# Performance work log

Measured on AMD Instinct MI355X. Metric: run time of the kernel, lower is better.

## Reference

```python
import jax, jax.numpy as jnp
import numpy as np

BATCH, D_MODEL, N_STATE, SEQ_L = 8, 1024, 64, 2048


def setup_inputs() -> dict:
    key = jax.random.key(0)
    k_u, k_a, k_b, k_c = jax.random.split(key, 4)
    scale = 1.0 / (D_MODEL * N_STATE) ** 0.5
    u = jax.random.normal(k_u, (BATCH, D_MODEL, SEQ_L), dtype=jnp.float32)
    # A is stored as a full NxN diagonal matrix, as in the torch module
    A = jnp.diag(jax.random.uniform(k_a, (N_STATE,), dtype=jnp.float32))
    B = jax.random.normal(k_b, (D_MODEL, N_STATE), dtype=jnp.float32) * scale
    C = jax.random.normal(k_c, (D_MODEL, N_STATE), dtype=jnp.float32) * scale
    return {"L": SEQ_L, "u": u, "A": A, "B": B, "C": C}


def reference(L, u, A, B, C):
    # u: (B, D, L). einsum('nn,bnd->bnd', A, h) in torch == diag(A) broadcast over h.
    a = jnp.diagonal(A)                       # (N,)
    Bu = jnp.einsum('dn,bdl->bnl', B, u)      # (B, N, L)
    Cu = jnp.einsum('dn,bdl->bnl', C, u)      # (B, N, L)
    bsz, d, _ = u.shape
    h0 = jnp.zeros((bsz, a.shape[0], d), dtype=u.dtype)  # (B, N, D)

    def step(h, xs):
        bu_l, cu_l, u_l = xs                  # (B,N), (B,N), (B,D)
        h = a[None, :, None] * h + bu_l[:, :, None] * u_l[:, None, :]
        y_l = jnp.einsum('bn,bnd->bd', cu_l, h)
        return h, y_l

    xs = (jnp.moveaxis(Bu, -1, 0), jnp.moveaxis(Cu, -1, 0), jnp.moveaxis(u, -1, 0))
    _, ys = jax.lax.scan(step, h0, xs)        # ys: (L, B, D)
    return jnp.moveaxis(ys, 0, -1)            # (B, D, L)
```

## Files before the change

### kernel.cpp

```cpp
#include <hip/hip_runtime.h>
#include <hip/hip_bf16.h>
#include <string.h>

#define BATCH 8
#define DM 1024
#define NS 64
#define SL 2048
#define NC 32
#define TC 64

typedef __attribute__((ext_vector_type(8))) short bf16x8;
typedef __attribute__((ext_vector_type(4))) float f32x4;
typedef float v2f __attribute__((ext_vector_type(2)));

__device__ inline unsigned short f2bf(float f) {
    union { float f; unsigned u; } v; v.f = f;
    return (unsigned short)((v.u + 0x7fffu + ((v.u >> 16) & 1u)) >> 16);
}
__device__ inline float bf2f(unsigned short h) {
    return __uint_as_float(((unsigned)h) << 16);
}
static __device__ inline v2f bfpair_to_v2f(unsigned int p) {
    unsigned int lo = p << 16, hi = p & 0xffff0000u;
    v2f r; r.x = __uint_as_float(lo); r.y = __uint_as_float(hi); return r;
}


__global__ __launch_bounds__(256) void k_prep(const float* __restrict__ Bm,
                                              const float* __restrict__ Cm,
                                              unsigned short* __restrict__ BT,
                                              unsigned short* __restrict__ CT)
{
    __shared__ float sT[64][65];
    const float* src = blockIdx.y ? Cm : Bm;
    unsigned short* dst = blockIdx.y ? CT : BT;
    const int d0 = blockIdx.x * 64, t = threadIdx.x;
    {
        int r = t >> 2, f = (t & 3) * 16;
#pragma unroll
        for (int i = 0; i < 4; i++) {
            float4 v = *(const float4*)&src[(size_t)(d0 + r) * NS + f + i * 4];
            sT[r][f + i * 4 + 0] = v.x; sT[r][f + i * 4 + 1] = v.y;
            sT[r][f + i * 4 + 2] = v.z; sT[r][f + i * 4 + 3] = v.w;
        }
    }
    __syncthreads();
    {
        int n = t >> 2, dq = (t & 3) * 16;
        unsigned pk[8];
#pragma unroll
        for (int k = 0; k < 8; k++) {
            unsigned short a = f2bf(sT[dq + 2 * k][n]);
            unsigned short bb = f2bf(sT[dq + 2 * k + 1][n]);
            pk[k] = (unsigned)a | ((unsigned)bb << 16);
        }
        uint4 v0 = { pk[0], pk[1], pk[2], pk[3] };
        uint4 v1 = { pk[4], pk[5], pk[6], pk[7] };
        *(uint4*)&dst[(size_t)n * DM + d0 + dq] = v0;
        *(uint4*)&dst[(size_t)n * DM + d0 + dq + 8] = v1;
    }
}

__global__ __launch_bounds__(512) void k_proj(const float* __restrict__ u,
                                              const unsigned short* __restrict__ BC,
                                              unsigned short* __restrict__ BuT,
                                              unsigned short* __restrict__ CuT)
{
    __shared__ unsigned short sA[32 * 64];
    __shared__ unsigned short sB[128 * 64];
    const int b = blockIdx.y, l0 = blockIdx.x * 32, t = threadIdx.x;
    const int lane = t & 63, w = t >> 6, g = lane >> 4, m15 = lane & 15;
    const int dd = t >> 3, c8 = t & 7;
    const int dq = dd >> 3, d7 = dd & 7;

    f32x4 acc[2];
    acc[0] = (f32x4){0.f, 0.f, 0.f, 0.f};
    acc[1] = (f32x4){0.f, 0.f, 0.f, 0.f};

#pragma unroll 1
    for (int d0 = 0; d0 < DM; d0 += 64) {
        __syncthreads();
        {
            float4 v = *(const float4*)&u[((size_t)b * DM + d0 + dd) * SL + l0 + c8 * 4];
            int l = c8 * 4;
            sA[(l + 0) * 64 + ((dq ^ ((l + 0) & 7)) * 8) + d7] = f2bf(v.x);
            sA[(l + 1) * 64 + ((dq ^ ((l + 1) & 7)) * 8) + d7] = f2bf(v.y);
            sA[(l + 2) * 64 + ((dq ^ ((l + 2) & 7)) * 8) + d7] = f2bf(v.z);
            sA[(l + 3) * 64 + ((dq ^ ((l + 3) & 7)) * 8) + d7] = f2bf(v.w);
        }
#pragma unroll
        for (int p = 0; p < 2; p++) {
            int idx = p * 512 + t;
            int row = idx >> 3, cc8 = idx & 7;
            uint4 v = *(const uint4*)(BC + (size_t)row * DM + d0 + cc8 * 8);
            *(uint4*)&sB[row * 64 + ((cc8 ^ (row & 7)) * 8)] = v;
        }
        __syncthreads();
#pragma unroll
        for (int ks = 0; ks < 2; ks++) {
            bf16x8 af[2], bfr;
#pragma unroll
            for (int mt = 0; mt < 2; mt++) {
                int r = mt * 16 + m15;
                af[mt] = *(const bf16x8*)&sA[r * 64 + (((ks * 4 + g) ^ (r & 7)) * 8)];
            }
            {
                int r = w * 16 + m15;
                bfr = *(const bf16x8*)&sB[r * 64 + (((ks * 4 + g) ^ (r & 7)) * 8)];
            }
#pragma unroll
            for (int mt = 0; mt < 2; mt++)
                acc[mt] = __builtin_amdgcn_mfma_f32_16x16x32_bf16(af[mt], bfr, acc[mt], 0, 0, 0);
        }
    }
    {
        int wn = w * 16 + m15;
        unsigned short* dst = (wn < 64) ? BuT : CuT;
        int n = wn & 63;
#pragma unroll
        for (int mt = 0; mt < 2; mt++)
#pragma unroll
            for (int r = 0; r < 4; r++) {
                int l = l0 + mt * 16 + g * 4 + r;
                dst[((size_t)b * SL + l) * NS + n] = f2bf(acc[mt][r]);
            }
    }
}

__global__ __launch_bounds__(256) void k_g(const float* __restrict__ A,
                                           const unsigned short* __restrict__ BuT,
                                           const unsigned short* __restrict__ CuT,
                                           unsigned short* __restrict__ Gw,
                                           unsigned short* __restrict__ Bvw,
                                           unsigned short* __restrict__ Wcw)
{
    __shared__ unsigned short sCu[64 * 64];
    __shared__ unsigned short sBu[8 * 64 * 8];
    __shared__ unsigned short sP[8 * 66 * 8];
    __shared__ unsigned short sTb[64 * 66];
    const int cc = blockIdx.x, b = cc >> 5, c = cc & 31;
    const int t = threadIdx.x, lane = t & 63;
    const int l0 = c * TC;
    const size_t gbase = (size_t)cc * 4096;

    {
        const unsigned short* srcC = CuT + ((size_t)b * SL + l0) * NS;
        const unsigned short* srcB = BuT + ((size_t)b * SL + l0) * NS;
#pragma unroll
        for (int p = 0; p < 2; p++) {
            int idx = p * 256 + t;
            int r = idx >> 3, q8 = idx & 7;
            uint4 vc = *(const uint4*)(srcC + (size_t)r * NS + q8 * 8);
            *(uint4*)&sCu[r * 64 + q8 * 8] = vc;
            uint4 vb = *(const uint4*)(srcB + (size_t)r * NS + q8 * 8);
            *(uint4*)&sBu[(q8 * 64 + r) * 8] = vb;
        }
    }
    {
        int n = t & 63;
        float an = A[n * NS + n];
        int q = n >> 3, n7 = n & 7;
#pragma unroll 1
        for (int dl = (t >> 6) * 17; dl < (t >> 6) * 17 + 17 && dl <= 64; dl++)
            sP[(q * 66 + dl) * 8 + n7] = f2bf(__powf(an, (float)dl));
    }
    __syncthreads();

#pragma unroll 1
    for (int r = 0; r < 16; r++) {
        int idx = r * 256 + t;
        int l = idx >> 6;
        int lp = lane;
        int dl = l - lp;
        float acc = 0.f;
        if (dl >= 0) {
#pragma unroll
            for (int q = 0; q < 8; q++) {
                bf16x8 cu = *(const bf16x8*)&sCu[l * 64 + q * 8];
                bf16x8 bu = *(const bf16x8*)&sBu[(q * 64 + lp) * 8];
                bf16x8 pp = *(const bf16x8*)&sP[(q * 66 + dl) * 8];
#pragma unroll
                for (int j = 0; j < 8; j++)
                    acc = fmaf(bf2f((unsigned short)cu[j]) * bf2f((unsigned short)bu[j]),
                               bf2f((unsigned short)pp[j]), acc);
            }
        }
        Gw[gbase + l * 64 + lp] = (dl >= 0) ? f2bf(acc) : (unsigned short)0;
    }

#pragma unroll 1
    for (int r = 0; r < 16; r++) {
        int idx = r * 256 + t;
        int l = idx >> 6;
        int n = lane, q = n >> 3, n7 = n & 7;
        float cu = bf2f(sCu[l * 64 + n]);
        float pv = bf2f(sP[(q * 66 + (l + 1)) * 8 + n7]);
        Wcw[gbase + l * 64 + n] = f2bf(cu * pv);
    }

#pragma unroll 1
    for (int r = 0; r < 16; r++) {
        int idx = r * 256 + t;
        int l = idx >> 6;
        int n = lane, q = n >> 3, n7 = n & 7;
        float bu = bf2f(sBu[(q * 64 + l) * 8 + n7]);
        float pv = bf2f(sP[(q * 66 + (63 - l)) * 8 + n7]);
        sTb[n * 66 + l] = f2bf(bu * pv);
    }
    __syncthreads();
#pragma unroll 1
    for (int r = 0; r < 16; r++) {
        int idx = r * 256 + t;
        int n = idx >> 6;
        int l = lane;
        Bvw[gbase + n * 64 + l] = sTb[n * 66 + l];
    }
}

__global__ __launch_bounds__(256) void k_state(const float* __restrict__ u,
                                               const unsigned short* __restrict__ Bvw,
                                               unsigned short* __restrict__ Ew)
{
    __shared__ unsigned short sU[256 * 64];
    __shared__ unsigned short sV[64 * 64];
    const int slab = blockIdx.x, c = blockIdx.y, b = blockIdx.z;
    const int d0 = slab * 256, l0 = c * TC;
    const int t = threadIdx.x, lane = t & 63, w = t >> 6, g = lane >> 4, m15 = lane & 15;

    {
        size_t gbase = ((size_t)(b * NC + c)) * 4096;
        int rr = t >> 3, c8 = t & 7;
#pragma unroll
        for (int p = 0; p < 2; p++) {
            int r = p * 32 + rr;
            uint4 vv = *(const uint4*)(Bvw + gbase + r * 64 + c8 * 8);
            *(uint4*)&sV[r * 64 + ((c8 ^ (r & 7)) * 8)] = vv;
        }
    }
#pragma unroll
    for (int p = 0; p < 16; p++) {
        int dd = p * 16 + (t >> 4), f = t & 15;
        float4 v = *(const float4*)&u[((size_t)b * DM + d0 + dd) * SL + l0 + f * 4];
        unsigned lo = (unsigned)f2bf(v.x) | ((unsigned)f2bf(v.y) << 16);
        unsigned hi = (unsigned)f2bf(v.z) | ((unsigned)f2bf(v.w) << 16);
        uint2 pk = { lo, hi };
        *(uint2*)&sU[dd * 64 + (((f >> 1) ^ (dd & 7)) * 8) + (f & 1) * 4] = pk;
    }
    __syncthreads();

    f32x4 accE[4][4];
#pragma unroll
    for (int i = 0; i < 4; i++)
#pragma unroll
        for (int j = 0; j < 4; j++) accE[i][j] = (f32x4){0.f, 0.f, 0.f, 0.f};

#pragma unroll
    for (int ks = 0; ks < 2; ks++) {
        bf16x8 af[4];
#pragma unroll
        for (int mt = 0; mt < 4; mt++) {
            int r = w * 64 + mt * 16 + m15;
            af[mt] = *(const bf16x8*)&sU[r * 64 + (((ks * 4 + g) ^ (r & 7)) * 8)];
        }
#pragma unroll
        for (int nt = 0; nt < 4; nt++) {
            int rg = nt * 16 + m15;
            bf16x8 bv = *(const bf16x8*)&sV[rg * 64 + (((ks * 4 + g) ^ (rg & 7)) * 8)];
#pragma unroll
            for (int mt = 0; mt < 4; mt++)
                accE[mt][nt] = __builtin_amdgcn_mfma_f32_16x16x32_bf16(af[mt], bv, accE[mt][nt], 0, 0, 0);
        }
    }
#pragma unroll
    for (int mt = 0; mt < 4; mt++)
#pragma unroll
        for (int nt = 0; nt < 4; nt++)
#pragma unroll
            for (int r = 0; r < 4; r++) {
                int d = d0 + w * 64 + mt * 16 + g * 4 + r;
                Ew[(((size_t)b * NC + c) * DM + d) * NS + nt * 16 + m15] = f2bf(accE[mt][nt][r]);
            }
}

__global__ __launch_bounds__(256) void k_prefix(const float* __restrict__ A,
                                                unsigned short* __restrict__ E)
{
    int gg = blockIdx.x * 256 + threadIdx.x;
    int p  = gg & 31;
    int d  = (gg >> 5) & (DM - 1);
    int b  = gg >> 15;
    int n0 = p * 2;

    float a0 = A[n0 * NS + n0];
    float a1 = A[(n0 + 1) * NS + (n0 + 1)];
    v2f aT = { __powf(a0, (float)TC), __powf(a1, (float)TC) };
    v2f hs = { 0.f, 0.f };

    unsigned int* base = (unsigned int*)E + ((((size_t)b * NC) * DM + d) * NS >> 1) + p;
    const size_t cstride = ((size_t)DM * NS) >> 1;

#pragma unroll 4
    for (int c = 0; c < NC; c++) {
        unsigned int* ptr = base + (size_t)c * cstride;
        unsigned int e = *ptr;
        unsigned int sw = (unsigned)f2bf(hs.x) | ((unsigned)f2bf(hs.y) << 16);
        *ptr = sw;
        hs = __builtin_elementwise_fma(aT, hs, bfpair_to_v2f(e));
    }
}

__global__ __launch_bounds__(256) void k_y(const float* __restrict__ u,
                                           const unsigned short* __restrict__ Gw,
                                           const unsigned short* __restrict__ Wcw,
                                           const unsigned short* __restrict__ HS,
                                           float* __restrict__ y)
{
    __shared__ unsigned short sU[256 * 64];
    __shared__ unsigned short sG[64 * 64];
    __shared__ unsigned short sW[64 * 64];
    const int slab = blockIdx.x, c = blockIdx.y, b = blockIdx.z;
    const int d0 = slab * 256, l0 = c * TC;
    const int t = threadIdx.x, lane = t & 63, w = t >> 6, g = lane >> 4, m15 = lane & 15;

    {
        size_t gbase = ((size_t)(b * NC + c)) * 4096;
        int rr = t >> 3, c8 = t & 7;
#pragma unroll
        for (int p = 0; p < 2; p++) {
            int r = p * 32 + rr;
            uint4 gv = *(const uint4*)(Gw + gbase + r * 64 + c8 * 8);
            *(uint4*)&sG[r * 64 + ((c8 ^ (r & 7)) * 8)] = gv;
            uint4 wv = *(const uint4*)(Wcw + gbase + r * 64 + c8 * 8);
            *(uint4*)&sW[r * 64 + ((c8 ^ (r & 7)) * 8)] = wv;
        }
    }
#pragma unroll
    for (int p = 0; p < 16; p++) {
        int dd = p * 16 + (t >> 4), f = t & 15;
        float4 v = *(const float4*)&u[((size_t)b * DM + d0 + dd) * SL + l0 + f * 4];
        unsigned lo = (unsigned)f2bf(v.x) | ((unsigned)f2bf(v.y) << 16);
        unsigned hi = (unsigned)f2bf(v.z) | ((unsigned)f2bf(v.w) << 16);
        uint2 pk = { lo, hi };
        *(uint2*)&sU[dd * 64 + (((f >> 1) ^ (dd & 7)) * 8) + (f & 1) * 4] = pk;
    }
    __syncthreads();

    f32x4 acc[4][4];
#pragma unroll
    for (int i = 0; i < 4; i++)
#pragma unroll
        for (int j = 0; j < 4; j++) acc[i][j] = (f32x4){0.f, 0.f, 0.f, 0.f};

    const unsigned short* hbase = HS + (((size_t)b * NC + c) * DM + d0) * NS;

#pragma unroll
    for (int ks = 0; ks < 2; ks++) {
        bf16x8 af[4];
#pragma unroll
        for (int mt = 0; mt < 4; mt++) {
            int r = w * 64 + mt * 16 + m15;
            af[mt] = *(const bf16x8*)&sU[r * 64 + (((ks * 4 + g) ^ (r & 7)) * 8)];
        }
#pragma unroll
        for (int nt = 0; nt < 4; nt++) {
            int rg = nt * 16 + m15;
            bf16x8 bg = *(const bf16x8*)&sG[rg * 64 + (((ks * 4 + g) ^ (rg & 7)) * 8)];
#pragma unroll
            for (int mt = 0; mt < 4; mt++)
                acc[mt][nt] = __builtin_amdgcn_mfma_f32_16x16x32_bf16(af[mt], bg, acc[mt][nt], 0, 0, 0);
        }
    }
#pragma unroll
    for (int ks = 0; ks < 2; ks++) {
        bf16x8 ah[4];
#pragma unroll
        for (int mt = 0; mt < 4; mt++) {
            int r = w * 64 + mt * 16 + m15;
            ah[mt] = *(const bf16x8*)(hbase + (size_t)r * NS + (ks * 4 + g) * 8);
        }
#pragma unroll
        for (int nt = 0; nt < 4; nt++) {
            int rg = nt * 16 + m15;
            bf16x8 bw = *(const bf16x8*)&sW[rg * 64 + (((ks * 4 + g) ^ (rg & 7)) * 8)];
#pragma unroll
            for (int mt = 0; mt < 4; mt++)
                acc[mt][nt] = __builtin_amdgcn_mfma_f32_16x16x32_bf16(ah[mt], bw, acc[mt][nt], 0, 0, 0);
        }
    }
#pragma unroll
    for (int mt = 0; mt < 4; mt++)
#pragma unroll
        for (int nt = 0; nt < 4; nt++)
#pragma unroll
            for (int r = 0; r < 4; r++) {
                int d = d0 + w * 64 + mt * 16 + g * 4 + r;
                int l = l0 + nt * 16 + m15;
                y[((size_t)b * DM + d) * SL + l] = acc[mt][nt][r];
            }
}

extern "C" void kernel_launch(void* const* d_in, const int* in_sizes, int n_in,
                              void* d_out, int out_size, void* d_ws, size_t ws_size,
                              hipStream_t stream) {
    const float* u = (const float*)d_in[1];
    const float* A = (const float*)d_in[2];
    const float* B = (const float*)d_in[3];
    const float* C = (const float*)d_in[4];
    float* y = (float*)d_out;

    char* base = (char*)d_ws;
    unsigned short* BuT = (unsigned short*)(base);
    unsigned short* CuT = (unsigned short*)(base + (2u << 20));
    unsigned short* BT  = (unsigned short*)(base + (4u << 20));
    unsigned short* Gw  = (unsigned short*)(base + (5u << 20));
    unsigned short* Bvw = (unsigned short*)(base + (7u << 20));
    unsigned short* Wcw = (unsigned short*)(base + (9u << 20));
    unsigned short* Ew  = (unsigned short*)(base + (11u << 20));
    unsigned short* CT  = BT + (size_t)NS * DM;

    k_prep<<<dim3(DM / 64, 2), 256, 0, stream>>>(B, C, BT, CT);
    k_proj<<<dim3(SL / 32, BATCH), 512, 0, stream>>>(u, BT, BuT, CuT);
    k_g<<<dim3(BATCH * NC), 256, 0, stream>>>(A, BuT, CuT, Gw, Bvw, Wcw);
    k_state<<<dim3(4, NC, BATCH), 256, 0, stream>>>(u, Bvw, Ew);
    k_prefix<<<dim3(BATCH * DM * 32 / 256), 256, 0, stream>>>(A, Ew);
    k_y<<<dim3(4, NC, BATCH), 256, 0, stream>>>(u, Gw, Wcw, Ew, y);
}
```

Before: 110.1 us.

## Cache bf16 copy of u in projection kernel and split k_g across two blocks

The projection kernel now also writes a bf16 copy of u to workspace, and the state and output kernels load this half-size copy instead of re-reading and converting fp32 u. The g-kernel grid gains a second dimension: each block computes half of the G rows, and the two blocks divide the Wcw and Bvw products between them. This cuts global memory reads of u and doubles block-level parallelism for k_g, at the cost of an extra write of the bf16 tensor and a larger workspace footprint.

```diff
diff --git a/kernel.cpp b/kernel.cpp
--- a/kernel.cpp
+++ b/kernel.cpp
@@ -64,7 +64,8 @@
 __global__ __launch_bounds__(512) void k_proj(const float* __restrict__ u,
                                               const unsigned short* __restrict__ BC,
                                               unsigned short* __restrict__ BuT,
-                                              unsigned short* __restrict__ CuT)
+                                              unsigned short* __restrict__ CuT,
+                                              unsigned short* __restrict__ Ubf)
 {
     __shared__ unsigned short sA[32 * 64];
     __shared__ unsigned short sB[128 * 64];
@@ -82,11 +83,15 @@
         __syncthreads();
         {
             float4 v = *(const float4*)&u[((size_t)b * DM + d0 + dd) * SL + l0 + c8 * 4];
+            unsigned short b0 = f2bf(v.x), b1 = f2bf(v.y), b2 = f2bf(v.z), b3 = f2bf(v.w);
             int l = c8 * 4;
-            sA[(l + 0) * 64 + ((dq ^ ((l + 0) & 7)) * 8) + d7] = f2bf(v.x);
-            sA[(l + 1) * 64 + ((dq ^ ((l + 1) & 7)) * 8) + d7] = f2bf(v.y);
-            sA[(l + 2) * 64 + ((dq ^ ((l + 2) & 7)) * 8) + d7] = f2bf(v.z);
-            sA[(l + 3) * 64 + ((dq ^ ((l + 3) & 7)) * 8) + d7] = f2bf(v.w);
+            sA[(l + 0) * 64 + ((dq ^ ((l + 0) & 7)) * 8) + d7] = b0;
+            sA[(l + 1) * 64 + ((dq ^ ((l + 1) & 7)) * 8) + d7] = b1;
+            sA[(l + 2) * 64 + ((dq ^ ((l + 2) & 7)) * 8) + d7] = b2;
+            sA[(l + 3) * 64 + ((dq ^ ((l + 3) & 7)) * 8) + d7] = b3;
+            uint2 pk = { (unsigned)b0 | ((unsigned)b1 << 16),
+                         (unsigned)b2 | ((unsigned)b3 << 16) };
+            *(uint2*)(Ubf + ((size_t)b * DM + d0 + dd) * SL + l0 + c8 * 4) = pk;
         }
 #pragma unroll
         for (int p = 0; p < 2; p++) {
@@ -139,6 +144,7 @@
     __shared__ unsigned short sP[8 * 66 * 8];
     __shared__ unsigned short sTb[64 * 66];
     const int cc = blockIdx.x, b = cc >> 5, c = cc & 31;
+    const int gy = blockIdx.y;
     const int t = threadIdx.x, lane = t & 63;
     const int l0 = c * TC;
     const size_t gbase = (size_t)cc * 4096;
@@ -167,7 +173,7 @@
     __syncthreads();
 
 #pragma unroll 1
-    for (int r = 0; r < 16; r++) {
+    for (int r = gy * 8; r < gy * 8 + 8; r++) {
         int idx = r * 256 + t;
         int l = idx >> 6;
         int lp = lane;
@@ -188,36 +194,38 @@
         Gw[gbase + l * 64 + lp] = (dl >= 0) ? f2bf(acc) : (unsigned short)0;
     }
 
-#pragma unroll 1
-    for (int r = 0; r < 16; r++) {
-        int idx = r * 256 + t;
-        int l = idx >> 6;
-        int n = lane, q = n >> 3, n7 = n & 7;
-        float cu = bf2f(sCu[l * 64 + n]);
-        float pv = bf2f(sP[(q * 66 + (l + 1)) * 8 + n7]);
-        Wcw[gbase + l * 64 + n] = f2bf(cu * pv);
-    }
-
-#pragma unroll 1
-    for (int r = 0; r < 16; r++) {
-        int idx = r * 256 + t;
-        int l = idx >> 6;
-        int n = lane, q = n >> 3, n7 = n & 7;
-        float bu = bf2f(sBu[(q * 64 + l) * 8 + n7]);
-        float pv = bf2f(sP[(q * 66 + (63 - l)) * 8 + n7]);
-        sTb[n * 66 + l] = f2bf(bu * pv);
-    }
-    __syncthreads();
-#pragma unroll 1
-    for (int r = 0; r < 16; r++) {
-        int idx = r * 256 + t;
-        int n = idx >> 6;
-        int l = lane;
-        Bvw[gbase + n * 64 + l] = sTb[n * 66 + l];
-    }
-}
-
-__global__ __launch_bounds__(256) void k_state(const float* __restrict__ u,
+    if (gy == 0) {
+#pragma unroll 1
+        for (int r = 0; r < 16; r++) {
+            int idx = r * 256 + t;
+            int l = idx >> 6;
+            int n = lane, q = n >> 3, n7 = n & 7;
+            float cu = bf2f(sCu[l * 64 + n]);
+            float pv = bf2f(sP[(q * 66 + (l + 1)) * 8 + n7]);
+            Wcw[gbase + l * 64 + n] = f2bf(cu * pv);
+        }
+    } else {
+#pragma unroll 1
+        for (int r = 0; r < 16; r++) {
+            int idx = r * 256 + t;
+            int l = idx >> 6;
+            int n = lane, q = n >> 3, n7 = n & 7;
+            float bu = bf2f(sBu[(q * 64 + l) * 8 + n7]);
+            float pv = bf2f(sP[(q * 66 + (63 - l)) * 8 + n7]);
+            sTb[n * 66 + l] = f2bf(bu * pv);
+        }
+        __syncthreads();
+#pragma unroll 1
+        for (int r = 0; r < 16; r++) {
+            int idx = r * 256 + t;
+            int n = idx >> 6;
+            int l = lane;
+            Bvw[gbase + n * 64 + l] = sTb[n * 66 + l];
+        }
+    }
+}
+
+__global__ __launch_bounds__(256) void k_state(const unsigned short* __restrict__ Ubf,
                                                const unsigned short* __restrict__ Bvw,
                                                unsigned short* __restrict__ Ew)
 {
@@ -237,14 +245,15 @@
             *(uint4*)&sV[r * 64 + ((c8 ^ (r & 7)) * 8)] = vv;
         }
     }
-#pragma unroll
-    for (int p = 0; p < 16; p++) {
-        int dd = p * 16 + (t >> 4), f = t & 15;
-        float4 v = *(const float4*)&u[((size_t)b * DM + d0 + dd) * SL + l0 + f * 4];
-        unsigned lo = (unsigned)f2bf(v.x) | ((unsigned)f2bf(v.y) << 16);
-        unsigned hi = (unsigned)f2bf(v.z) | ((unsigned)f2bf(v.w) << 16);
-        uint2 pk = { lo, hi };
-        *(uint2*)&sU[dd * 64 + (((f >> 1) ^ (dd & 7)) * 8) + (f & 1) * 4] = pk;
+    {
+        const unsigned short* usrc = Ubf + ((size_t)b * DM + d0) * SL + l0;
+#pragma unroll
+        for (int p = 0; p < 8; p++) {
+            int idx = p * 256 + t;
+            int dd = idx >> 3, q8 = idx & 7;
+            uint4 v = *(const uint4*)(usrc + (size_t)dd * SL + q8 * 8);
+            *(uint4*)&sU[dd * 64 + ((q8 ^ (dd & 7)) * 8)] = v;
+        }
     }
     __syncthreads();
 
@@ -309,7 +318,7 @@
     }
 }
 
-__global__ __launch_bounds__(256) void k_y(const float* __restrict__ u,
+__global__ __launch_bounds__(256) void k_y(const unsigned short* __restrict__ Ubf,
                                            const unsigned short* __restrict__ Gw,
                                            const unsigned short* __restrict__ Wcw,
                                            const unsigned short* __restrict__ HS,
@@ -334,14 +343,15 @@
             *(uint4*)&sW[r * 64 + ((c8 ^ (r & 7)) * 8)] = wv;
         }
     }
-#pragma unroll
-    for (int p = 0; p < 16; p++) {
-        int dd = p * 16 + (t >> 4), f = t & 15;
-        float4 v = *(const float4*)&u[((size_t)b * DM + d0 + dd) * SL + l0 + f * 4];
-        unsigned lo = (unsigned)f2bf(v.x) | ((unsigned)f2bf(v.y) << 16);
-        unsigned hi = (unsigned)f2bf(v.z) | ((unsigned)f2bf(v.w) << 16);
-        uint2 pk = { lo, hi };
-        *(uint2*)&sU[dd * 64 + (((f >> 1) ^ (dd & 7)) * 8) + (f & 1) * 4] = pk;
+    {
+        const unsigned short* usrc = Ubf + ((size_t)b * DM + d0) * SL + l0;
+#pragma unroll
+        for (int p = 0; p < 8; p++) {
+            int idx = p * 256 + t;
+            int dd = idx >> 3, q8 = idx & 7;
+            uint4 v = *(const uint4*)(usrc + (size_t)dd * SL + q8 * 8);
+            *(uint4*)&sU[dd * 64 + ((q8 ^ (dd & 7)) * 8)] = v;
+        }
     }
     __syncthreads();
 
@@ -416,12 +426,13 @@
     unsigned short* Bvw = (unsigned short*)(base + (7u << 20));
     unsigned short* Wcw = (unsigned short*)(base + (9u << 20));
     unsigned short* Ew  = (unsigned short*)(base + (11u << 20));
+    unsigned short* Ubf = (unsigned short*)(base + (44u << 20));
     unsigned short* CT  = BT + (size_t)NS * DM;
 
     k_prep<<<dim3(DM / 64, 2), 256, 0, stream>>>(B, C, BT, CT);
-    k_proj<<<dim3(SL / 32, BATCH), 512, 0, stream>>>(u, BT, BuT, CuT);
-    k_g<<<dim3(BATCH * NC), 256, 0, stream>>>(A, BuT, CuT, Gw, Bvw, Wcw);
-    k_state<<<dim3(4, NC, BATCH), 256, 0, stream>>>(u, Bvw, Ew);
+    k_proj<<<dim3(SL / 32, BATCH), 512, 0, stream>>>(u, BT, BuT, CuT, Ubf);
+    k_g<<<dim3(BATCH * NC, 2), 256, 0, stream>>>(A, BuT, CuT, Gw, Bvw, Wcw);
+    k_state<<<dim3(4, NC, BATCH), 256, 0, stream>>>(Ubf, Bvw, Ew);
     k_prefix<<<dim3(BATCH * DM * 32 / 256), 256, 0, stream>>>(A, Ew);
-    k_y<<<dim3(4, NC, BATCH), 256, 0, stream>>>(u, Gw, Wcw, Ew, y);
-}
+    k_y<<<dim3(4, NC, BATCH), 256, 0, stream>>>(Ubf, Gw, Wcw, Ew, y);
+}
```

Measured after the change: 104.0 us, median of 2. -5.6%, faster.
